# Performance work log

Measured on AMD Instinct MI355X. Metric: run time of the kernel, lower is better.

Reference implementation:

```python
import jax, jax.numpy as jnp
import numpy as np

EPS = 1e-5
SLOPE = 0.2

def _leaky(x):
    return jnp.where(x >= 0, x, SLOPE * x)

def _bn(x, g, b, axes):
    # batch-norm in training mode: biased stats over `axes`, per remaining channel dim
    mu = jnp.mean(x, axis=axes, keepdims=True)
    var = jnp.var(x, axis=axes, keepdims=True)
    shape = [1] * x.ndim
    shape[2 if x.ndim == 5 else 1] = -1
    return (x - mu) * jax.lax.rsqrt(var + EPS) * g.reshape(shape) + b.reshape(shape)

def setup_inputs() -> dict:
    key = jax.random.key(0)
    ks = jax.random.split(key, 6)
    T, B, C, H, W, D = 17, 16, 512, 16, 16, 256
    return {
        "cond": jax.random.normal(ks[0], (B, D), jnp.float32),
        "xbar": jax.random.normal(ks[1], (T, B, C, H, W), jnp.float32),
        "lin_w": jax.random.normal(ks[2], (D, D), jnp.float32) * 0.05,
        "lin_b": jnp.zeros((D,), jnp.float32),
        "bn_s_g": jnp.ones((D,), jnp.float32),
        "bn_s_b": jnp.zeros((D,), jnp.float32),
        "conv1_w": jax.random.normal(ks[3], (C, C), jnp.float32) * 0.05,
        "bn1_g": jnp.ones((C,), jnp.float32),
        "bn1_b": jnp.zeros((C,), jnp.float32),
        "conv2_w": jax.random.normal(ks[4], (C, C + D), jnp.float32) * 0.05,
        "bn2_g": jnp.ones((C,), jnp.float32),
        "bn2_b": jnp.zeros((C,), jnp.float32),
        "conv3_w": jax.random.normal(ks[5], (1, C, 2, 2), jnp.float32) * 0.05,
    }

def reference(cond, xbar, lin_w, lin_b, bn_s_g, bn_s_b, conv1_w, bn1_g, bn1_b, conv2_w, bn2_g, bn2_b, conv3_w):
    # sent_map: Linear -> BatchNorm1d (over batch) -> LeakyReLU
    sent = cond @ lin_w.T + lin_b                       # [B, D]
    sent = _leaky(_bn(sent, bn_s_g, bn_s_b, axes=(0,)))

    motions = xbar[1:] - xbar[:-1]                      # [F, B, C, H, W]
    F, B, C, H, W = motions.shape

    # motion_map: 1x1 conv -> BN (per-frame stats, matching the python loop) -> LeakyReLU
    h = jnp.einsum('fbchw,oc->fbohw', motions, conv1_w)
    h = _leaky(_bn(h, bn1_g, bn1_b, axes=(1, 3, 4)))

    # broadcast sentence vector over space (replaces per-pixel python loop)
    sent_dupe = jnp.broadcast_to(sent[None, :, :, None, None], (F, B, sent.shape[1], H, W))
    ms = jnp.concatenate([h, sent_dupe], axis=2)        # [F, B, C+D, H, W]

    # predictor: 1x1 conv -> BN (per-frame) -> LeakyReLU -> 2x2 stride-2 conv
    h2 = jnp.einsum('fbchw,oc->fbohw', ms, conv2_w)
    h2 = _leaky(_bn(h2, bn2_g, bn2_b, axes=(1, 3, 4)))

    h2f = h2.reshape(F * B, C, H, W)
    out = jax.lax.conv_general_dilated(
        h2f, conv3_w, window_strides=(2, 2), padding='VALID',
        dimension_numbers=('NCHW', 'OIHW', 'NCHW'))     # [F*B, 1, H/2, W/2]
    return out.reshape(F, B, -1)                        # matches view(B,-1) per frame + stack
```

## Files before the change

### kernel.cpp

```cpp
#include <hip/hip_runtime.h>
#include <hip/hip_bf16.h>

#define EPS 1e-5f
#define SLOPE 0.2f

#define NF 16
#define NBATCH 16
#define NC 512
#define NHW 256
#define ND 256
#define K2 768
#define MF 4096
#define FRAME_ELEMS ((size_t)MF * NC)

typedef __attribute__((ext_vector_type(8))) short short8;
typedef __attribute__((ext_vector_type(4))) float float4v;

__device__ __forceinline__ float lrelu(float v) { return v >= 0.f ? v : SLOPE * v; }
__device__ __forceinline__ float b2f(ushort u) { union { float f; uint i; } x; x.i = ((uint)u) << 16; return x.f; }
__device__ __forceinline__ ushort f2b(float f) {
  uint i = __float_as_uint(f);
  return (ushort)((i + 0x7FFFu + ((i >> 16) & 1u)) >> 16);
}
__device__ __forceinline__ void gl16(const ushort* g, ushort* l) {
  __builtin_amdgcn_global_load_lds(
      (const __attribute__((address_space(1))) unsigned int*)g,
      (__attribute__((address_space(3))) unsigned int*)l, 16, 0, 0);
}
#define SB __builtin_amdgcn_sched_barrier(0)

__global__ __launch_bounds__(256) void k_pre(
    const float* __restrict__ w1, const float* __restrict__ w2,
    const float* __restrict__ cond, const float* __restrict__ lin_w,
    const float* __restrict__ lin_b, const float* __restrict__ gam,
    const float* __restrict__ bet,
    ushort* __restrict__ w1b, ushort* __restrict__ w2b,
    float* __restrict__ bias2) {
  int bx = blockIdx.x, t = threadIdx.x;
  if (bx < 1024) {
    int i = bx * 256 + t;
    w1b[i] = f2b(w1[i]);
    int o = i >> 9, c = i & 511;
    w2b[i] = f2b(w2[(size_t)o * K2 + c]);
    return;
  }
  __shared__ float sl[NBATCH][ND];
  int d = t;
  {
    float acc[NBATCH];
    float bias = lin_b[d];
#pragma unroll
    for (int b = 0; b < NBATCH; ++b) acc[b] = bias;
    for (int k = 0; k < ND; ++k) {
      float w = lin_w[d * ND + k];
#pragma unroll
      for (int b = 0; b < NBATCH; ++b) acc[b] = fmaf(cond[b * ND + k], w, acc[b]);
    }
    float mu = 0.f;
#pragma unroll
    for (int b = 0; b < NBATCH; ++b) mu += acc[b];
    mu *= (1.f / NBATCH);
    float var = 0.f;
#pragma unroll
    for (int b = 0; b < NBATCH; ++b) { float x = acc[b] - mu; var = fmaf(x, x, var); }
    var *= (1.f / NBATCH);
    float sc = rsqrtf(var + EPS) * gam[d];
    float sh = bet[d] - mu * sc;
#pragma unroll
    for (int b = 0; b < NBATCH; ++b) sl[b][d] = lrelu(fmaf(acc[b], sc, sh));
  }
  __syncthreads();
  int o = (bx - 1024) * 256 + t;
  float acc2[NBATCH];
#pragma unroll
  for (int b = 0; b < NBATCH; ++b) acc2[b] = 0.f;
  for (int d2 = 0; d2 < ND; ++d2) {
    float wv = w2[(size_t)o * K2 + NC + d2];
#pragma unroll
    for (int b = 0; b < NBATCH; ++b) acc2[b] = fmaf(sl[b][d2], wv, acc2[b]);
  }
#pragma unroll
  for (int b = 0; b < NBATCH; ++b) bias2[b * NC + o] = acc2[b];
}

__device__ __forceinline__ void gemm_epi(
    float4v (&acc)[8][4], ushort* lds, const float* bias2, int has_bias,
    ushort* __restrict__ H, float2* __restrict__ part,
    int g, int bx, int n0, int w, int l, int wr, int wc) {
  int m0 = bx * 256;
  float bz[4];
#pragma unroll
  for (int fn = 0; fn < 4; ++fn)
    bz[fn] = has_bias ? bias2[bx * NC + n0 + wc * 64 + fn * 16 + (l & 15)] : 0.f;
  float sv[4], qv[4];
#pragma unroll
  for (int fn = 0; fn < 4; ++fn) {
    float s = 0.f, q = 0.f;
#pragma unroll
    for (int fm = 0; fm < 8; ++fm)
#pragma unroll
      for (int j = 0; j < 4; ++j) {
        float v = acc[fm][fn][j] + bz[fn];
        acc[fm][fn][j] = v;
        s += v;
        q = fmaf(v, v, q);
      }
    s += __shfl_xor(s, 16); s += __shfl_xor(s, 32);
    q += __shfl_xor(q, 16); q += __shfl_xor(q, 32);
    sv[fn] = s; qv[fn] = q;
  }
  if (l < 16) {
    int mb = bx * 2 + wr;
    float2* pp = part + ((size_t)g * 32 + mb) * NC + n0 + wc * 64 + l;
#pragma unroll
    for (int fn = 0; fn < 4; ++fn) pp[fn * 16] = make_float2(sv[fn], qv[fn]);
  }
  ushort* ep = &lds[w * 1088];
  ushort* Hg = H + ((size_t)g * MF + m0 + wr * 128) * NC + n0 + wc * 64;
#pragma unroll
  for (int fm = 0; fm < 8; ++fm) {
#pragma unroll
    for (int fn = 0; fn < 4; ++fn)
#pragma unroll
      for (int j = 0; j < 4; ++j)
        ep[((l >> 4) * 4 + j) * 68 + fn * 16 + (l & 15)] = f2b(acc[fm][fn][j]);
#pragma unroll
    for (int h = 0; h < 2; ++h) {
      int r = h * 8 + (l >> 3), sl = l & 7;
      short8 v = *(const short8*)&ep[r * 68 + sl * 8];
      *(short8*)&Hg[(size_t)(fm * 16 + r) * NC + sl * 8] = v;
    }
  }
}

__global__ __launch_bounds__(512, 2) void k_gemm1f(
    const float* __restrict__ xbar, const ushort* __restrict__ W,
    ushort* __restrict__ H, float2* __restrict__ part, int f0) {
  __shared__ ushort lds[65536];
  const int t = threadIdx.x, w = t >> 6, l = t & 63;
  const int g = blockIdx.z, bx = blockIdx.x, ny = blockIdx.y;
  const int n0 = ny * 256;
  const int wr = w >> 2, wc = w & 3;

  const ushort* Wg = W + (size_t)n0 * NC;
  size_t goff[4];
  int loff[4];
#pragma unroll
  for (int q = 0; q < 4; ++q) {
    int u = w * 256 + q * 64 + l;
    int row = u >> 3, cb = (u & 7) ^ (row & 7);
    goff[q] = (size_t)row * NC + cb * 8;
    loff[q] = u * 8;
  }
  const float* x0 = xbar + (((size_t)(f0 + g) * NBATCH + bx) * NC + w * 8) * NHW + l * 4;
  const float* x1 = x0 + (size_t)NBATCH * NC * NHW;

  int slot[2];
#pragma unroll
  for (int kk = 0; kk < 2; ++kk) slot[kk] = (((kk * 4 + (l >> 4)) ^ (l & 7)) * 8);
  const int swbase = w;

  float4 p0[4], p1[4];
#define AISSUE(h_, kt_)                                                      \
  do {                                                                       \
    _Pragma("unroll") for (int cc = 0; cc < 4; ++cc) {                       \
      size_t off = (size_t)((kt_) * 64 + (h_) * 4 + cc) * NHW;               \
      p1[cc] = *(const float4*)(x1 + off);                                   \
      p0[cc] = *(const float4*)(x0 + off);                                   \
    }                                                                        \
  } while (0)
#define ATRANS(h_, b_)                                                       \
  do {                                                                       \
    _Pragma("unroll") for (int i = 0; i < 4; ++i) {                          \
      int hw = l * 4 + i;                                                    \
      uint lo = (uint)f2b(((const float*)&p1[0])[i] - ((const float*)&p0[0])[i]) | \
                ((uint)f2b(((const float*)&p1[1])[i] - ((const float*)&p0[1])[i]) << 16); \
      uint hi = (uint)f2b(((const float*)&p1[2])[i] - ((const float*)&p0[2])[i]) | \
                ((uint)f2b(((const float*)&p1[3])[i] - ((const float*)&p0[3])[i]) << 16); \
      uint2 pk = make_uint2(lo, hi);                                         \
      *(uint2*)&lds[(b_) * 32768 + hw * 64 + ((swbase ^ (hw & 7)) * 8) + (h_) * 4] = pk; \
    }                                                                        \
  } while (0)
#define WSTAGE(t_, b_)                                                       \
  do {                                                                       \
    _Pragma("unroll") for (int q = 0; q < 4; ++q)                            \
        gl16(Wg + goff[q] + (t_) * 64, &lds[(b_) * 32768 + 16384 + loff[q]]); \
  } while (0)

  AISSUE(0, 0);
  WSTAGE(0, 0);
  WSTAGE(1, 1);
  asm volatile("s_waitcnt vmcnt(0)" ::: "memory"); SB;
  ATRANS(0, 0);
  AISSUE(1, 0);
  asm volatile("s_waitcnt vmcnt(0)" ::: "memory"); SB;
  ATRANS(1, 0);
  asm volatile("s_waitcnt lgkmcnt(0)" ::: "memory"); SB;
  __builtin_amdgcn_s_barrier(); SB;

  float4v acc[8][4];
#pragma unroll
  for (int i = 0; i < 8; ++i)
#pragma unroll
    for (int j = 0; j < 4; ++j) acc[i][j] = (float4v)0.f;

#pragma unroll
  for (int kt = 0; kt < 8; ++kt) {
    const int cur = kt & 1;
    const ushort* la = &lds[cur * 32768];
    const ushort* lb = la + 16384;
    if (kt < 7) AISSUE(0, kt + 1);
    short8 bf[4][2], af[4][2];
#pragma unroll
    for (int fn = 0; fn < 4; ++fn) {
      int r = wc * 64 + fn * 16 + (l & 15);
#pragma unroll
      for (int kk = 0; kk < 2; ++kk) bf[fn][kk] = *(const short8*)&lb[r * 64 + slot[kk]];
    }
#pragma unroll
    for (int fm = 0; fm < 4; ++fm) {
      int r = wr * 128 + fm * 16 + (l & 15);
#pragma unroll
      for (int kk = 0; kk < 2; ++kk) af[fm][kk] = *(const short8*)&la[r * 64 + slot[kk]];
    }
    asm volatile("s_waitcnt lgkmcnt(0)" ::: "memory"); SB;
    __builtin_amdgcn_s_setprio(1);
#pragma unroll
    for (int kk = 0; kk < 2; ++kk)
#pragma unroll
      for (int fm = 0; fm < 4; ++fm)
#pragma unroll
        for (int fn = 0; fn < 4; ++fn)
          acc[fm][fn] = __builtin_amdgcn_mfma_f32_16x16x32_bf16(
              af[fm][kk], bf[fn][kk], acc[fm][fn], 0, 0, 0);
    __builtin_amdgcn_s_setprio(0);
#pragma unroll
    for (int fm = 0; fm < 4; ++fm) {
      int r = wr * 128 + 64 + fm * 16 + (l & 15);
#pragma unroll
      for (int kk = 0; kk < 2; ++kk) af[fm][kk] = *(const short8*)&la[r * 64 + slot[kk]];
    }
    asm volatile("s_waitcnt lgkmcnt(0)" ::: "memory"); SB;
    __builtin_amdgcn_s_barrier(); SB;
    if (kt < 7) {
      asm volatile("s_waitcnt vmcnt(0)" ::: "memory"); SB;
      ATRANS(0, cur ^ 1);
      AISSUE(1, kt + 1);
      asm volatile("s_waitcnt vmcnt(0)" ::: "memory"); SB;
      ATRANS(1, cur ^ 1);
    }
    if (kt < 6) WSTAGE(kt + 2, cur);
    __builtin_amdgcn_s_setprio(1);
#pragma unroll
    for (int kk = 0; kk < 2; ++kk)
#pragma unroll
      for (int fm = 0; fm < 4; ++fm)
#pragma unroll
        for (int fn = 0; fn < 4; ++fn)
          acc[fm + 4][fn] = __builtin_amdgcn_mfma_f32_16x16x32_bf16(
              af[fm][kk], bf[fn][kk], acc[fm + 4][fn], 0, 0, 0);
    __builtin_amdgcn_s_setprio(0);
    if (kt < 7) {
      asm volatile("s_waitcnt lgkmcnt(0)" ::: "memory"); SB;
      __builtin_amdgcn_s_barrier(); SB;
    }
  }
#undef AISSUE
#undef ATRANS
#undef WSTAGE
  SB; __builtin_amdgcn_s_barrier(); SB;
  gemm_epi(acc, lds, nullptr, 0, H, part, g, bx, n0, w, l, wr, wc);
}

__global__ __launch_bounds__(512, 2) void k_gemm2f(
    const ushort* __restrict__ A, const ushort* __restrict__ W,
    const float2* __restrict__ st, const float* __restrict__ bias2,
    ushort* __restrict__ H, float2* __restrict__ part) {
  __shared__ ushort lds[65536];
  __shared__ float2 stl[NC];
  const int t = threadIdx.x, w = t >> 6, l = t & 63;
  const int g = blockIdx.z, bx = blockIdx.x, ny = blockIdx.y;
  const int m0 = bx * 256, n0 = ny * 256;
  const int wr = w >> 2, wc = w & 3;

  const ushort* Wg = W + (size_t)n0 * NC;
  const ushort* Ab = A + ((size_t)g * MF + m0) * NC;
  size_t goff[4], agoff[4];
  int loff[4], arow[4];
#pragma unroll
  for (int q = 0; q < 4; ++q) {
    int u = w * 256 + q * 64 + l;
    int row = u >> 3, cb = (u & 7) ^ (row & 7);
    goff[q] = (size_t)row * NC + cb * 8;
    loff[q] = u * 8;
    arow[q] = row;
    agoff[q] = (size_t)row * NC + (l & 7) * 8;
  }
  int slot[2];
#pragma unroll
  for (int kk = 0; kk < 2; ++kk) slot[kk] = (((kk * 4 + (l >> 4)) ^ (l & 7)) * 8);

  short8 ar[4];
  float2 sr[8];
#define A2ISSUE(kt_)                                                         \
  do {                                                                       \
    _Pragma("unroll") for (int q = 0; q < 4; ++q)                            \
        ar[q] = *(const short8*)(Ab + agoff[q] + (kt_) * 64);                \
  } while (0)
#define SRREAD(kt_)                                                          \
  do {                                                                       \
    _Pragma("unroll") for (int e = 0; e < 8; ++e)                            \
        sr[e] = stl[(kt_) * 64 + (l & 7) * 8 + e];                           \
  } while (0)
#define A2TRANS(b_)                                                          \
  do {                                                                       \
    _Pragma("unroll") for (int q = 0; q < 4; ++q) {                          \
      uint out[4];                                                           \
      _Pragma("unroll") for (int j = 0; j < 4; ++j) {                        \
        float xa = fmaf(b2f((ushort)ar[q][2 * j]), sr[2 * j].x, sr[2 * j].y); \
        float xb = fmaf(b2f((ushort)ar[q][2 * j + 1]), sr[2 * j + 1].x, sr[2 * j + 1].y); \
        xa = fmaxf(xa, SLOPE * xa);                                          \
        xb = fmaxf(xb, SLOPE * xb);                                          \
        out[j] = (uint)f2b(xa) | ((uint)f2b(xb) << 16);                      \
      }                                                                      \
      *(uint4*)&lds[(b_) * 32768 + arow[q] * 64 + (((l & 7) ^ (arow[q] & 7)) * 8)] = \
          *(const uint4*)out;                                                \
    }                                                                        \
  } while (0)
#define WSTAGE2(t_, b_)                                                      \
  do {                                                                       \
    _Pragma("unroll") for (int q = 0; q < 4; ++q)                            \
        gl16(Wg + goff[q] + (t_) * 64, &lds[(b_) * 32768 + 16384 + loff[q]]); \
  } while (0)

  stl[t] = st[(size_t)g * NC + t];
  if (t + 512 < NC) {}
  A2ISSUE(0);
  WSTAGE2(0, 0);
  WSTAGE2(1, 1);
  asm volatile("s_waitcnt lgkmcnt(0)" ::: "memory"); SB;
  __builtin_amdgcn_s_barrier(); SB;
  SRREAD(0);
  asm volatile("s_waitcnt vmcnt(0) lgkmcnt(0)" ::: "memory"); SB;
  A2TRANS(0);
  asm volatile("s_waitcnt lgkmcnt(0)" ::: "memory"); SB;
  __builtin_amdgcn_s_barrier(); SB;

  float4v acc[8][4];
#pragma unroll
  for (int i = 0; i < 8; ++i)
#pragma unroll
    for (int j = 0; j < 4; ++j) acc[i][j] = (float4v)0.f;

#pragma unroll
  for (int kt = 0; kt < 8; ++kt) {
    const int cur = kt & 1;
    const ushort* la = &lds[cur * 32768];
    const ushort* lb = la + 16384;
    if (kt < 7) A2ISSUE(kt + 1);
    short8 bf[4][2], af[4][2];
#pragma unroll
    for (int fn = 0; fn < 4; ++fn) {
      int r = wc * 64 + fn * 16 + (l & 15);
#pragma unroll
      for (int kk = 0; kk < 2; ++kk) bf[fn][kk] = *(const short8*)&lb[r * 64 + slot[kk]];
    }
#pragma unroll
    for (int fm = 0; fm < 4; ++fm) {
      int r = wr * 128 + fm * 16 + (l & 15);
#pragma unroll
      for (int kk = 0; kk < 2; ++kk) af[fm][kk] = *(const short8*)&la[r * 64 + slot[kk]];
    }
    asm volatile("s_waitcnt lgkmcnt(0)" ::: "memory"); SB;
    __builtin_amdgcn_s_setprio(1);
#pragma unroll
    for (int kk = 0; kk < 2; ++kk)
#pragma unroll
      for (int fm = 0; fm < 4; ++fm)
#pragma unroll
        for (int fn = 0; fn < 4; ++fn)
          acc[fm][fn] = __builtin_amdgcn_mfma_f32_16x16x32_bf16(
              af[fm][kk], bf[fn][kk], acc[fm][fn], 0, 0, 0);
    __builtin_amdgcn_s_setprio(0);
#pragma unroll
    for (int fm = 0; fm < 4; ++fm) {
      int r = wr * 128 + 64 + fm * 16 + (l & 15);
#pragma unroll
      for (int kk = 0; kk < 2; ++kk) af[fm][kk] = *(const short8*)&la[r * 64 + slot[kk]];
    }
    asm volatile("s_waitcnt lgkmcnt(0)" ::: "memory"); SB;
    __builtin_amdgcn_s_barrier(); SB;
    if (kt < 7) {
      SRREAD(kt + 1);
      asm volatile("s_waitcnt vmcnt(0) lgkmcnt(0)" ::: "memory"); SB;
      A2TRANS(cur ^ 1);
    }
    if (kt < 6) WSTAGE2(kt + 2, cur);
    __builtin_amdgcn_s_setprio(1);
#pragma unroll
    for (int kk = 0; kk < 2; ++kk)
#pragma unroll
      for (int fm = 0; fm < 4; ++fm)
#pragma unroll
        for (int fn = 0; fn < 4; ++fn)
          acc[fm + 4][fn] = __builtin_amdgcn_mfma_f32_16x16x32_bf16(
              af[fm][kk], bf[fn][kk], acc[fm + 4][fn], 0, 0, 0);
    __builtin_amdgcn_s_setprio(0);
    if (kt < 7) {
      asm volatile("s_waitcnt lgkmcnt(0)" ::: "memory"); SB;
      __builtin_amdgcn_s_barrier(); SB;
    }
  }
#undef A2ISSUE
#undef SRREAD
#undef A2TRANS
#undef WSTAGE2
  SB; __builtin_amdgcn_s_barrier(); SB;
  gemm_epi(acc, lds, bias2, 1, H, part, g, bx, n0, w, l, wr, wc);
}

__global__ __launch_bounds__(256) void k_stats2(
    const float2* __restrict__ part, const float* __restrict__ gam,
    const float* __restrict__ bet, float2* __restrict__ st) {
  int bi = blockIdx.x;
  int g = bi >> 1;
  int o = (bi & 1) * 256 + threadIdx.x;
  float s = 0.f, q = 0.f;
#pragma unroll
  for (int mb = 0; mb < 32; ++mb) {
    float2 v = part[((size_t)g * 32 + mb) * NC + o];
    s += v.x;
    q += v.y;
  }
  float mu = s * (1.f / 4096.f);
  float var = q * (1.f / 4096.f) - mu * mu;
  float sc = rsqrtf(var + EPS) * gam[o];
  st[g * NC + o] = make_float2(sc, bet[o] - mu * sc);
}

__global__ __launch_bounds__(256) void k_conv3(
    const ushort* __restrict__ h2, const float2* __restrict__ st2,
    const float* __restrict__ w3, float* __restrict__ out, int f0) {
  int g = blockIdx.z;
  int b = blockIdx.x >> 2;
  int q = blockIdx.x & 3;
  int t = threadIdx.x;
  int oi = q * 16 + (t >> 4);
  int cs = t & 15;
  int y = oi >> 3, x = oi & 7;
  const ushort* base = h2 + ((size_t)g * MF + b * NHW) * NC;
  int m00 = (2 * y) * 16 + 2 * x;
  float acc = 0.f;
#pragma unroll
  for (int c8 = cs * 32; c8 < cs * 32 + 32; c8 += 8) {
    short8 v0 = *(const short8*)&base[(size_t)(m00 + 0) * NC + c8];
    short8 v1 = *(const short8*)&base[(size_t)(m00 + 1) * NC + c8];
    short8 v2 = *(const short8*)&base[(size_t)(m00 + 16) * NC + c8];
    short8 v3 = *(const short8*)&base[(size_t)(m00 + 17) * NC + c8];
#pragma unroll
    for (int e = 0; e < 8; ++e) {
      float2 ss = st2[g * NC + c8 + e];
      float4 wv = ((const float4*)w3)[c8 + e];
      acc = fmaf(lrelu(fmaf(b2f((ushort)v0[e]), ss.x, ss.y)), wv.x, acc);
      acc = fmaf(lrelu(fmaf(b2f((ushort)v1[e]), ss.x, ss.y)), wv.y, acc);
      acc = fmaf(lrelu(fmaf(b2f((ushort)v2[e]), ss.x, ss.y)), wv.z, acc);
      acc = fmaf(lrelu(fmaf(b2f((ushort)v3[e]), ss.x, ss.y)), wv.w, acc);
    }
  }
  acc += __shfl_xor(acc, 1);
  acc += __shfl_xor(acc, 2);
  acc += __shfl_xor(acc, 4);
  acc += __shfl_xor(acc, 8);
  if (cs == 0) out[((size_t)(f0 + g) * NBATCH + b) * 64 + oi] = acc;
}

extern "C" void kernel_launch(void* const* d_in, const int* in_sizes, int n_in,
                              void* d_out, int out_size, void* d_ws, size_t ws_size,
                              hipStream_t stream) {
  const float* cond = (const float*)d_in[0];
  const float* xbar = (const float*)d_in[1];
  const float* lin_w = (const float*)d_in[2];
  const float* lin_b = (const float*)d_in[3];
  const float* bnsg = (const float*)d_in[4];
  const float* bnsb = (const float*)d_in[5];
  const float* w1 = (const float*)d_in[6];
  const float* bn1g = (const float*)d_in[7];
  const float* bn1b = (const float*)d_in[8];
  const float* w2 = (const float*)d_in[9];
  const float* bn2g = (const float*)d_in[10];
  const float* bn2b = (const float*)d_in[11];
  const float* w3 = (const float*)d_in[12];
  float* out = (float*)d_out;

  char* p = (char*)d_ws;
  float* bias2 = (float*)p;   p += ((NBATCH * NC * 4 + 255) & ~255);
  float2* st1 = (float2*)p;   p += ((NF * NC * 8 + 255) & ~255);
  float2* st2 = (float2*)p;   p += ((NF * NC * 8 + 255) & ~255);
  float2* part = (float2*)p;  p += (((size_t)NF * 32 * NC * 8 + 255) & ~255);
  ushort* w1b = (ushort*)p;   p += ((NC * NC * 2 + 255) & ~255);
  ushort* w2b = (ushort*)p;   p += ((NC * NC * 2 + 255) & ~255);
  size_t used = (size_t)(p - (char*)d_ws);
  const size_t frame_bytes = FRAME_ELEMS * 2;
  size_t rem = ws_size > used ? ws_size - used : 0;
  int FB = (int)(rem / (2 * frame_bytes));
  if (FB < 1) FB = 1;
  if (FB > NF) FB = NF;
  ushort* bufB = (ushort*)p;
  ushort* bufC = bufB + (size_t)FB * FRAME_ELEMS;

  k_pre<<<1026, 256, 0, stream>>>(w1, w2, cond, lin_w, lin_b, bnsg, bnsb,
                                  w1b, w2b, bias2);

  for (int f0 = 0; f0 < NF; f0 += FB) {
    int nb = (NF - f0) < FB ? (NF - f0) : FB;
    k_gemm1f<<<dim3(16, 2, nb), 512, 0, stream>>>(xbar, w1b, bufB, part, f0);
    k_stats2<<<2 * nb, 256, 0, stream>>>(part, bn1g, bn1b, st1);
    k_gemm2f<<<dim3(16, 2, nb), 512, 0, stream>>>(bufB, w2b, st1, bias2, bufC, part);
    k_stats2<<<2 * nb, 256, 0, stream>>>(part, bn2g, bn2b, st2);
    k_conv3<<<dim3(NBATCH * 4, 1, nb), 256, 0, stream>>>(bufC, st2, w3, out, f0);
  }
}
```

Before: 313.6 us.

## Split frame-difference transpose into separate kernel feeding a plain bf16 GEMM

Unfuses motion computation from the first GEMM. A new kernel computes consecutive-frame differences, converts them to bf16 and transposes them to channel-last, streaming each xbar frame once across a group of four frames instead of reading every frame twice. The first GEMM then loads both A and W tiles with direct global-to-LDS copies in a clean double-buffered pipeline, with no register transpose. The cost is an extra bf16 intermediate buffer written and read back, plus a third workspace buffer that may shrink the frame batch size.

```diff
diff --git a/kernel.cpp b/kernel.cpp
--- a/kernel.cpp
+++ b/kernel.cpp
@@ -83,6 +83,58 @@
   for (int b = 0; b < NBATCH; ++b) bias2[b * NC + o] = acc2[b];
 }
 
+__global__ __launch_bounds__(256) void k_mot(
+    const float* __restrict__ xbar, ushort* __restrict__ mot, int f0, int nb) {
+  __shared__ ushort T2[64][72];
+  int t = threadIdx.x;
+  int b = blockIdx.y;
+  int hw0 = (blockIdx.x & 3) * 64;
+  int c0 = (blockIdx.x >> 2) * 64;
+  int fg = blockIdx.z * 4;
+  int fe = fg + 4 < nb ? fg + 4 : nb;
+
+  int c4 = t >> 4;
+  int h16 = t & 15;
+  const size_t fstride = (size_t)NBATCH * NC * NHW;
+  const float* base = xbar + ((size_t)(f0 + fg) * NBATCH + b) * (NC * NHW) +
+                      (size_t)(c0 + c4 * 4) * NHW + hw0 + h16 * 4;
+
+  float4 prev[4], cur[4], nxt[4];
+#pragma unroll
+  for (int r = 0; r < 4; ++r) prev[r] = *(const float4*)(base + (size_t)r * NHW);
+#pragma unroll
+  for (int r = 0; r < 4; ++r) cur[r] = *(const float4*)(base + fstride + (size_t)r * NHW);
+
+  for (int fr = fg; fr < fe; ++fr) {
+    if (fr + 1 < fe) {
+      const float* xn = base + (size_t)(fr - fg + 2) * fstride;
+#pragma unroll
+      for (int r = 0; r < 4; ++r) nxt[r] = *(const float4*)(xn + (size_t)r * NHW);
+    }
+#pragma unroll
+    for (int i = 0; i < 4; ++i) {
+      ushort4 pk = make_ushort4(
+          f2b(((const float*)&cur[0])[i] - ((const float*)&prev[0])[i]),
+          f2b(((const float*)&cur[1])[i] - ((const float*)&prev[1])[i]),
+          f2b(((const float*)&cur[2])[i] - ((const float*)&prev[2])[i]),
+          f2b(((const float*)&cur[3])[i] - ((const float*)&prev[3])[i]));
+      *(ushort4*)&T2[h16 * 4 + i][c4 * 4] = pk;
+    }
+    __syncthreads();
+    ushort* mp = mot + ((size_t)fr * MF + b * NHW + hw0) * NC + c0;
+#pragma unroll
+    for (int it = 0; it < 2; ++it) {
+      int unit = it * 256 + t;
+      int hw = unit >> 3, q = unit & 7;
+      short8 v = *(const short8*)&T2[hw][q * 8];
+      *(short8*)&mp[(size_t)hw * NC + q * 8] = v;
+    }
+    __syncthreads();
+#pragma unroll
+    for (int r = 0; r < 4; ++r) { prev[r] = cur[r]; cur[r] = nxt[r]; }
+  }
+}
+
 __device__ __forceinline__ void gemm_epi(
     float4v (&acc)[8][4], ushort* lds, const float* bias2, int has_bias,
     ushort* __restrict__ H, float2* __restrict__ part,
@@ -133,16 +185,18 @@
   }
 }
 
-__global__ __launch_bounds__(512, 2) void k_gemm1f(
-    const float* __restrict__ xbar, const ushort* __restrict__ W,
-    ushort* __restrict__ H, float2* __restrict__ part, int f0) {
+__global__ __launch_bounds__(512, 2) void k_gemm8(
+    const ushort* __restrict__ A, const ushort* __restrict__ W,
+    ushort* __restrict__ H, float2* __restrict__ part) {
   __shared__ ushort lds[65536];
   const int t = threadIdx.x, w = t >> 6, l = t & 63;
   const int g = blockIdx.z, bx = blockIdx.x, ny = blockIdx.y;
-  const int n0 = ny * 256;
+  const int m0 = bx * 256, n0 = ny * 256;
   const int wr = w >> 2, wc = w & 3;
 
+  const ushort* Ag = A + (size_t)g * FRAME_ELEMS + (size_t)m0 * NC;
   const ushort* Wg = W + (size_t)n0 * NC;
+
   size_t goff[4];
   int loff[4];
 #pragma unroll
@@ -152,76 +206,50 @@
     goff[q] = (size_t)row * NC + cb * 8;
     loff[q] = u * 8;
   }
-  const float* x0 = xbar + (((size_t)(f0 + g) * NBATCH + bx) * NC + w * 8) * NHW + l * 4;
-  const float* x1 = x0 + (size_t)NBATCH * NC * NHW;
+
+#define STAGE8(t_, b_)                                               \
+  do {                                                               \
+    const int k0_ = (t_) * 64;                                       \
+    _Pragma("unroll") for (int q = 0; q < 4; ++q)                    \
+        gl16(Ag + goff[q] + k0_, &lds[(b_) * 32768 + loff[q]]);      \
+    _Pragma("unroll") for (int q = 0; q < 4; ++q)                    \
+        gl16(Wg + goff[q] + k0_, &lds[(b_) * 32768 + 16384 + loff[q]]); \
+  } while (0)
 
   int slot[2];
 #pragma unroll
   for (int kk = 0; kk < 2; ++kk) slot[kk] = (((kk * 4 + (l >> 4)) ^ (l & 7)) * 8);
-  const int swbase = w;
-
-  float4 p0[4], p1[4];
-#define AISSUE(h_, kt_)                                                      \
-  do {                                                                       \
-    _Pragma("unroll") for (int cc = 0; cc < 4; ++cc) {                       \
-      size_t off = (size_t)((kt_) * 64 + (h_) * 4 + cc) * NHW;               \
-      p1[cc] = *(const float4*)(x1 + off);                                   \
-      p0[cc] = *(const float4*)(x0 + off);                                   \
-    }                                                                        \
-  } while (0)
-#define ATRANS(h_, b_)                                                       \
-  do {                                                                       \
-    _Pragma("unroll") for (int i = 0; i < 4; ++i) {                          \
-      int hw = l * 4 + i;                                                    \
-      uint lo = (uint)f2b(((const float*)&p1[0])[i] - ((const float*)&p0[0])[i]) | \
-                ((uint)f2b(((const float*)&p1[1])[i] - ((const float*)&p0[1])[i]) << 16); \
-      uint hi = (uint)f2b(((const float*)&p1[2])[i] - ((const float*)&p0[2])[i]) | \
-                ((uint)f2b(((const float*)&p1[3])[i] - ((const float*)&p0[3])[i]) << 16); \
-      uint2 pk = make_uint2(lo, hi);                                         \
-      *(uint2*)&lds[(b_) * 32768 + hw * 64 + ((swbase ^ (hw & 7)) * 8) + (h_) * 4] = pk; \
-    }                                                                        \
-  } while (0)
-#define WSTAGE(t_, b_)                                                       \
-  do {                                                                       \
-    _Pragma("unroll") for (int q = 0; q < 4; ++q)                            \
-        gl16(Wg + goff[q] + (t_) * 64, &lds[(b_) * 32768 + 16384 + loff[q]]); \
-  } while (0)
-
-  AISSUE(0, 0);
-  WSTAGE(0, 0);
-  WSTAGE(1, 1);
-  asm volatile("s_waitcnt vmcnt(0)" ::: "memory"); SB;
-  ATRANS(0, 0);
-  AISSUE(1, 0);
-  asm volatile("s_waitcnt vmcnt(0)" ::: "memory"); SB;
-  ATRANS(1, 0);
-  asm volatile("s_waitcnt lgkmcnt(0)" ::: "memory"); SB;
+
+  float4v acc[8][4];
+#pragma unroll
+  for (int i = 0; i < 8; ++i)
+#pragma unroll
+    for (int j = 0; j < 4; ++j) acc[i][j] = (float4v)0.f;
+
+  STAGE8(0, 0);
+  STAGE8(1, 1);
+  asm volatile("s_waitcnt vmcnt(8)" ::: "memory"); SB;
   __builtin_amdgcn_s_barrier(); SB;
 
-  float4v acc[8][4];
-#pragma unroll
-  for (int i = 0; i < 8; ++i)
-#pragma unroll
-    for (int j = 0; j < 4; ++j) acc[i][j] = (float4v)0.f;
-
 #pragma unroll
   for (int kt = 0; kt < 8; ++kt) {
-    const int cur = kt & 1;
-    const ushort* la = &lds[cur * 32768];
+    const int b = kt & 1;
+    const ushort* la = &lds[b * 32768];
     const ushort* lb = la + 16384;
-    if (kt < 7) AISSUE(0, kt + 1);
     short8 bf[4][2], af[4][2];
 #pragma unroll
     for (int fn = 0; fn < 4; ++fn) {
       int r = wc * 64 + fn * 16 + (l & 15);
 #pragma unroll
-      for (int kk = 0; kk < 2; ++kk) bf[fn][kk] = *(const short8*)&lb[r * 64 + slot[kk]];
+      for (int kk = 0; kk < 2; ++kk)
+        bf[fn][kk] = *(const short8*)&lb[r * 64 + slot[kk]];
     }
 #pragma unroll
     for (int fm = 0; fm < 4; ++fm) {
       int r = wr * 128 + fm * 16 + (l & 15);
 #pragma unroll
-      for (int kk = 0; kk < 2; ++kk) af[fm][kk] = *(const short8*)&la[r * 64 + slot[kk]];
+      for (int kk = 0; kk < 2; ++kk)
+        af[fm][kk] = *(const short8*)&la[r * 64 + slot[kk]];
     }
     asm volatile("s_waitcnt lgkmcnt(0)" ::: "memory"); SB;
     __builtin_amdgcn_s_setprio(1);
@@ -238,18 +266,12 @@
     for (int fm = 0; fm < 4; ++fm) {
       int r = wr * 128 + 64 + fm * 16 + (l & 15);
 #pragma unroll
-      for (int kk = 0; kk < 2; ++kk) af[fm][kk] = *(const short8*)&la[r * 64 + slot[kk]];
+      for (int kk = 0; kk < 2; ++kk)
+        af[fm][kk] = *(const short8*)&la[r * 64 + slot[kk]];
     }
     asm volatile("s_waitcnt lgkmcnt(0)" ::: "memory"); SB;
     __builtin_amdgcn_s_barrier(); SB;
-    if (kt < 7) {
-      asm volatile("s_waitcnt vmcnt(0)" ::: "memory"); SB;
-      ATRANS(0, cur ^ 1);
-      AISSUE(1, kt + 1);
-      asm volatile("s_waitcnt vmcnt(0)" ::: "memory"); SB;
-      ATRANS(1, cur ^ 1);
-    }
-    if (kt < 6) WSTAGE(kt + 2, cur);
+    if (kt < 6) STAGE8(kt + 2, b);
     __builtin_amdgcn_s_setprio(1);
 #pragma unroll
     for (int kk = 0; kk < 2; ++kk)
@@ -261,13 +283,14 @@
               af[fm][kk], bf[fn][kk], acc[fm + 4][fn], 0, 0, 0);
     __builtin_amdgcn_s_setprio(0);
     if (kt < 7) {
-      asm volatile("s_waitcnt lgkmcnt(0)" ::: "memory"); SB;
+      if (kt < 6) asm volatile("s_waitcnt vmcnt(8)" ::: "memory");
+      else        asm volatile("s_waitcnt vmcnt(0)" ::: "memory");
+      SB;
       __builtin_amdgcn_s_barrier(); SB;
     }
   }
-#undef AISSUE
-#undef ATRANS
-#undef WSTAGE
+#undef STAGE8
+
   SB; __builtin_amdgcn_s_barrier(); SB;
   gemm_epi(acc, lds, nullptr, 0, H, part, g, bx, n0, w, l, wr, wc);
 }
@@ -334,7 +357,6 @@
   } while (0)
 
   stl[t] = st[(size_t)g * NC + t];
-  if (t + 512 < NC) {}
   A2ISSUE(0);
   WSTAGE2(0, 0);
   WSTAGE2(1, 1);
@@ -502,10 +524,11 @@
   size_t used = (size_t)(p - (char*)d_ws);
   const size_t frame_bytes = FRAME_ELEMS * 2;
   size_t rem = ws_size > used ? ws_size - used : 0;
-  int FB = (int)(rem / (2 * frame_bytes));
+  int FB = (int)(rem / (3 * frame_bytes));
   if (FB < 1) FB = 1;
   if (FB > NF) FB = NF;
-  ushort* bufB = (ushort*)p;
+  ushort* bufA = (ushort*)p;
+  ushort* bufB = bufA + (size_t)FB * FRAME_ELEMS;
   ushort* bufC = bufB + (size_t)FB * FRAME_ELEMS;
 
   k_pre<<<1026, 256, 0, stream>>>(w1, w2, cond, lin_w, lin_b, bnsg, bnsb,
@@ -513,7 +536,9 @@
 
   for (int f0 = 0; f0 < NF; f0 += FB) {
     int nb = (NF - f0) < FB ? (NF - f0) : FB;
-    k_gemm1f<<<dim3(16, 2, nb), 512, 0, stream>>>(xbar, w1b, bufB, part, f0);
+    int ngrp = (nb + 3) / 4;
+    k_mot<<<dim3(32, NBATCH, ngrp), 256, 0, stream>>>(xbar, bufA, f0, nb);
+    k_gemm8<<<dim3(16, 2, nb), 512, 0, stream>>>(bufA, w1b, bufB, part);
     k_stats2<<<2 * nb, 256, 0, stream>>>(part, bn1g, bn1b, st1);
     k_gemm2f<<<dim3(16, 2, nb), 512, 0, stream>>>(bufB, w2b, st1, bias2, bufC, part);
     k_stats2<<<2 * nb, 256, 0, stream>>>(part, bn2g, bn2b, st2);
```

After: 271.2 us. 13.5% less time.

## Restructure GEMM pipelines for deeper prefetch and single-barrier iterations

Applied to the files above, without the earlier changes.

Both GEMM kernels now prefetch the A operand two k-tiles ahead in registers (double register buffers in gemm2, a full 64-channel tile per ALD in gemm1), stage W one tile ahead instead of two, and drop the mid-iteration barrier, using partial vmcnt waits. gemm1 also changes its thread-to-channel/pixel mapping and swaps grid axes so the two N-blocks of the same frame/batch launch adjacently, which may improve L2 reuse of xbar. Launch bounds drop to 1 block per CU minimum, allowing more registers at the risk of lower occupancy.

```diff
diff --git a/kernel.cpp b/kernel.cpp
--- a/kernel.cpp
+++ b/kernel.cpp
@@ -133,13 +133,13 @@
   }
 }
 
-__global__ __launch_bounds__(512, 2) void k_gemm1f(
+__global__ __launch_bounds__(512, 1) void k_gemm1m(
     const float* __restrict__ xbar, const ushort* __restrict__ W,
     ushort* __restrict__ H, float2* __restrict__ part, int f0) {
   __shared__ ushort lds[65536];
   const int t = threadIdx.x, w = t >> 6, l = t & 63;
-  const int g = blockIdx.z, bx = blockIdx.x, ny = blockIdx.y;
-  const int n0 = ny * 256;
+  const int g = blockIdx.z, bx = blockIdx.y;
+  const int n0 = blockIdx.x * 256;
   const int wr = w >> 2, wc = w & 3;
 
   const ushort* Wg = W + (size_t)n0 * NC;
@@ -152,64 +152,65 @@
     goff[q] = (size_t)row * NC + cb * 8;
     loff[q] = u * 8;
   }
-  const float* x0 = xbar + (((size_t)(f0 + g) * NBATCH + bx) * NC + w * 8) * NHW + l * 4;
-  const float* x1 = x0 + (size_t)NBATCH * NC * NHW;
+#define WST(t_, b_)                                                      \
+  do {                                                                   \
+    _Pragma("unroll") for (int q = 0; q < 4; ++q)                        \
+        gl16(Wg + goff[q] + (t_) * 64, &lds[(b_) * 32768 + 16384 + loff[q]]); \
+  } while (0)
+
+  const int c4 = (t >> 3) & 15;
+  const int hh = ((t >> 7) << 3) + (t & 7);
+  const float* xb0 = xbar + ((size_t)(f0 + g) * NBATCH + bx) * (NC * NHW);
+  const float* xb1 = xb0 + (size_t)NBATCH * NC * NHW;
+
+  float4 pA[2][2][4];
+#define ALD(kt_)                                                         \
+  do {                                                                   \
+    _Pragma("unroll") for (int u = 0; u < 2; ++u)                        \
+      _Pragma("unroll") for (int cc = 0; cc < 4; ++cc) {                 \
+        size_t co = (size_t)((kt_) * 64 + c4 * 4 + cc) * NHW + hh * 4 + u * 128; \
+        pA[u][0][cc] = *(const float4*)(xb1 + co);                       \
+        pA[u][1][cc] = *(const float4*)(xb0 + co);                       \
+      }                                                                  \
+  } while (0)
+#define ATRANS(b_)                                                       \
+  do {                                                                   \
+    _Pragma("unroll") for (int u = 0; u < 2; ++u)                        \
+      _Pragma("unroll") for (int i = 0; i < 4; ++i) {                    \
+        int hw = hh * 4 + i + u * 128;                                   \
+        uint lo = (uint)f2b(((const float*)&pA[u][0][0])[i] - ((const float*)&pA[u][1][0])[i]) | \
+                  ((uint)f2b(((const float*)&pA[u][0][1])[i] - ((const float*)&pA[u][1][1])[i]) << 16); \
+        uint hi = (uint)f2b(((const float*)&pA[u][0][2])[i] - ((const float*)&pA[u][1][2])[i]) | \
+                  ((uint)f2b(((const float*)&pA[u][0][3])[i] - ((const float*)&pA[u][1][3])[i]) << 16); \
+        *(uint2*)&lds[(b_) * 32768 + hw * 64 + (((c4 >> 1) ^ (hw & 7)) * 8) + (c4 & 1) * 4] = \
+            make_uint2(lo, hi);                                          \
+      }                                                                  \
+  } while (0)
 
   int slot[2];
 #pragma unroll
   for (int kk = 0; kk < 2; ++kk) slot[kk] = (((kk * 4 + (l >> 4)) ^ (l & 7)) * 8);
-  const int swbase = w;
-
-  float4 p0[4], p1[4];
-#define AISSUE(h_, kt_)                                                      \
-  do {                                                                       \
-    _Pragma("unroll") for (int cc = 0; cc < 4; ++cc) {                       \
-      size_t off = (size_t)((kt_) * 64 + (h_) * 4 + cc) * NHW;               \
-      p1[cc] = *(const float4*)(x1 + off);                                   \
-      p0[cc] = *(const float4*)(x0 + off);                                   \
-    }                                                                        \
-  } while (0)
-#define ATRANS(h_, b_)                                                       \
-  do {                                                                       \
-    _Pragma("unroll") for (int i = 0; i < 4; ++i) {                          \
-      int hw = l * 4 + i;                                                    \
-      uint lo = (uint)f2b(((const float*)&p1[0])[i] - ((const float*)&p0[0])[i]) | \
-                ((uint)f2b(((const float*)&p1[1])[i] - ((const float*)&p0[1])[i]) << 16); \
-      uint hi = (uint)f2b(((const float*)&p1[2])[i] - ((const float*)&p0[2])[i]) | \
-                ((uint)f2b(((const float*)&p1[3])[i] - ((const float*)&p0[3])[i]) << 16); \
-      uint2 pk = make_uint2(lo, hi);                                         \
-      *(uint2*)&lds[(b_) * 32768 + hw * 64 + ((swbase ^ (hw & 7)) * 8) + (h_) * 4] = pk; \
-    }                                                                        \
-  } while (0)
-#define WSTAGE(t_, b_)                                                       \
-  do {                                                                       \
-    _Pragma("unroll") for (int q = 0; q < 4; ++q)                            \
-        gl16(Wg + goff[q] + (t_) * 64, &lds[(b_) * 32768 + 16384 + loff[q]]); \
-  } while (0)
-
-  AISSUE(0, 0);
-  WSTAGE(0, 0);
-  WSTAGE(1, 1);
-  asm volatile("s_waitcnt vmcnt(0)" ::: "memory"); SB;
-  ATRANS(0, 0);
-  AISSUE(1, 0);
-  asm volatile("s_waitcnt vmcnt(0)" ::: "memory"); SB;
-  ATRANS(1, 0);
+
+  float4v acc[8][4];
+#pragma unroll
+  for (int i = 0; i < 8; ++i)
+#pragma unroll
+    for (int j = 0; j < 4; ++j) acc[i][j] = (float4v)0.f;
+
+  ALD(0);
+  WST(0, 0);
+  asm volatile("s_waitcnt vmcnt(4)" ::: "memory"); SB;
+  ATRANS(0);
+  ALD(1);
   asm volatile("s_waitcnt lgkmcnt(0)" ::: "memory"); SB;
+  asm volatile("s_waitcnt vmcnt(16)" ::: "memory"); SB;
   __builtin_amdgcn_s_barrier(); SB;
-
-  float4v acc[8][4];
-#pragma unroll
-  for (int i = 0; i < 8; ++i)
-#pragma unroll
-    for (int j = 0; j < 4; ++j) acc[i][j] = (float4v)0.f;
 
 #pragma unroll
   for (int kt = 0; kt < 8; ++kt) {
     const int cur = kt & 1;
     const ushort* la = &lds[cur * 32768];
     const ushort* lb = la + 16384;
-    if (kt < 7) AISSUE(0, kt + 1);
     short8 bf[4][2], af[4][2];
 #pragma unroll
     for (int fn = 0; fn < 4; ++fn) {
@@ -241,15 +242,12 @@
       for (int kk = 0; kk < 2; ++kk) af[fm][kk] = *(const short8*)&la[r * 64 + slot[kk]];
     }
     asm volatile("s_waitcnt lgkmcnt(0)" ::: "memory"); SB;
-    __builtin_amdgcn_s_barrier(); SB;
     if (kt < 7) {
       asm volatile("s_waitcnt vmcnt(0)" ::: "memory"); SB;
-      ATRANS(0, cur ^ 1);
-      AISSUE(1, kt + 1);
-      asm volatile("s_waitcnt vmcnt(0)" ::: "memory"); SB;
-      ATRANS(1, cur ^ 1);
-    }
-    if (kt < 6) WSTAGE(kt + 2, cur);
+      ATRANS(cur ^ 1);
+      WST(kt + 1, cur ^ 1);
+      if (kt < 6) ALD(kt + 2);
+    }
     __builtin_amdgcn_s_setprio(1);
 #pragma unroll
     for (int kk = 0; kk < 2; ++kk)
@@ -262,17 +260,20 @@
     __builtin_amdgcn_s_setprio(0);
     if (kt < 7) {
       asm volatile("s_waitcnt lgkmcnt(0)" ::: "memory"); SB;
+      if (kt < 6) asm volatile("s_waitcnt vmcnt(16)" ::: "memory");
+      else        asm volatile("s_waitcnt vmcnt(0)" ::: "memory");
+      SB;
       __builtin_amdgcn_s_barrier(); SB;
     }
   }
-#undef AISSUE
+#undef ALD
 #undef ATRANS
-#undef WSTAGE
+#undef WST
   SB; __builtin_amdgcn_s_barrier(); SB;
   gemm_epi(acc, lds, nullptr, 0, H, part, g, bx, n0, w, l, wr, wc);
 }
 
-__global__ __launch_bounds__(512, 2) void k_gemm2f(
+__global__ __launch_bounds__(512, 1) void k_gemm2f(
     const ushort* __restrict__ A, const ushort* __restrict__ W,
     const float2* __restrict__ st, const float* __restrict__ bias2,
     ushort* __restrict__ H, float2* __restrict__ part) {
@@ -300,50 +301,50 @@
 #pragma unroll
   for (int kk = 0; kk < 2; ++kk) slot[kk] = (((kk * 4 + (l >> 4)) ^ (l & 7)) * 8);
 
-  short8 ar[4];
+  short8 ar0[4], ar1[4];
   float2 sr[8];
-#define A2ISSUE(kt_)                                                         \
-  do {                                                                       \
-    _Pragma("unroll") for (int q = 0; q < 4; ++q)                            \
-        ar[q] = *(const short8*)(Ab + agoff[q] + (kt_) * 64);                \
-  } while (0)
-#define SRREAD(kt_)                                                          \
-  do {                                                                       \
-    _Pragma("unroll") for (int e = 0; e < 8; ++e)                            \
-        sr[e] = stl[(kt_) * 64 + (l & 7) * 8 + e];                           \
-  } while (0)
-#define A2TRANS(b_)                                                          \
-  do {                                                                       \
-    _Pragma("unroll") for (int q = 0; q < 4; ++q) {                          \
-      uint out[4];                                                           \
-      _Pragma("unroll") for (int j = 0; j < 4; ++j) {                        \
-        float xa = fmaf(b2f((ushort)ar[q][2 * j]), sr[2 * j].x, sr[2 * j].y); \
-        float xb = fmaf(b2f((ushort)ar[q][2 * j + 1]), sr[2 * j + 1].x, sr[2 * j + 1].y); \
-        xa = fmaxf(xa, SLOPE * xa);                                          \
-        xb = fmaxf(xb, SLOPE * xb);                                          \
-        out[j] = (uint)f2b(xa) | ((uint)f2b(xb) << 16);                      \
-      }                                                                      \
+#define A2LD(kt_, dst)                                                   \
+  do {                                                                   \
+    _Pragma("unroll") for (int q = 0; q < 4; ++q)                        \
+        dst[q] = *(const short8*)(Ab + agoff[q] + (kt_) * 64);           \
+  } while (0)
+#define SRREAD(kt_)                                                      \
+  do {                                                                   \
+    _Pragma("unroll") for (int e = 0; e < 8; ++e)                        \
+        sr[e] = stl[(kt_) * 64 + (l & 7) * 8 + e];                       \
+  } while (0)
+#define A2TRANS(src, b_)                                                 \
+  do {                                                                   \
+    _Pragma("unroll") for (int q = 0; q < 4; ++q) {                      \
+      uint out[4];                                                       \
+      _Pragma("unroll") for (int j = 0; j < 4; ++j) {                    \
+        float xa = fmaf(b2f((ushort)src[q][2 * j]), sr[2 * j].x, sr[2 * j].y); \
+        float xb = fmaf(b2f((ushort)src[q][2 * j + 1]), sr[2 * j + 1].x, sr[2 * j + 1].y); \
+        xa = fmaxf(xa, SLOPE * xa);                                      \
+        xb = fmaxf(xb, SLOPE * xb);                                      \
+        out[j] = (uint)f2b(xa) | ((uint)f2b(xb) << 16);                  \
+      }                                                                  \
       *(uint4*)&lds[(b_) * 32768 + arow[q] * 64 + (((l & 7) ^ (arow[q] & 7)) * 8)] = \
-          *(const uint4*)out;                                                \
-    }                                                                        \
-  } while (0)
-#define WSTAGE2(t_, b_)                                                      \
-  do {                                                                       \
-    _Pragma("unroll") for (int q = 0; q < 4; ++q)                            \
+          *(const uint4*)out;                                            \
+    }                                                                    \
+  } while (0)
+#define WST2(t_, b_)                                                     \
+  do {                                                                   \
+    _Pragma("unroll") for (int q = 0; q < 4; ++q)                        \
         gl16(Wg + goff[q] + (t_) * 64, &lds[(b_) * 32768 + 16384 + loff[q]]); \
   } while (0)
 
   stl[t] = st[(size_t)g * NC + t];
-  if (t + 512 < NC) {}
-  A2ISSUE(0);
-  WSTAGE2(0, 0);
-  WSTAGE2(1, 1);
+  A2LD(0, ar0);
+  WST2(0, 0);
+  A2LD(1, ar1);
+  __syncthreads();
+  SRREAD(0);
+  asm volatile("s_waitcnt vmcnt(8)" ::: "memory"); SB;
   asm volatile("s_waitcnt lgkmcnt(0)" ::: "memory"); SB;
-  __builtin_amdgcn_s_barrier(); SB;
-  SRREAD(0);
-  asm volatile("s_waitcnt vmcnt(0) lgkmcnt(0)" ::: "memory"); SB;
-  A2TRANS(0);
+  A2TRANS(ar0, 0);
   asm volatile("s_waitcnt lgkmcnt(0)" ::: "memory"); SB;
+  asm volatile("s_waitcnt vmcnt(4)" ::: "memory"); SB;
   __builtin_amdgcn_s_barrier(); SB;
 
   float4v acc[8][4];
@@ -357,7 +358,7 @@
     const int cur = kt & 1;
     const ushort* la = &lds[cur * 32768];
     const ushort* lb = la + 16384;
-    if (kt < 7) A2ISSUE(kt + 1);
+    if (kt < 7) SRREAD(kt + 1);
     short8 bf[4][2], af[4][2];
 #pragma unroll
     for (int fn = 0; fn < 4; ++fn) {
@@ -389,13 +390,12 @@
       for (int kk = 0; kk < 2; ++kk) af[fm][kk] = *(const short8*)&la[r * 64 + slot[kk]];
     }
     asm volatile("s_waitcnt lgkmcnt(0)" ::: "memory"); SB;
-    __builtin_amdgcn_s_barrier(); SB;
     if (kt < 7) {
-      SRREAD(kt + 1);
-      asm volatile("s_waitcnt vmcnt(0) lgkmcnt(0)" ::: "memory"); SB;
-      A2TRANS(cur ^ 1);
-    }
-    if (kt < 6) WSTAGE2(kt + 2, cur);
+      asm volatile("s_waitcnt vmcnt(0)" ::: "memory"); SB;
+      if ((kt & 1) == 0) A2TRANS(ar1, cur ^ 1); else A2TRANS(ar0, cur ^ 1);
+      WST2(kt + 1, cur ^ 1);
+      if (kt < 6) { if ((kt & 1) == 0) A2LD(kt + 2, ar0); else A2LD(kt + 2, ar1); }
+    }
     __builtin_amdgcn_s_setprio(1);
 #pragma unroll
     for (int kk = 0; kk < 2; ++kk)
@@ -408,13 +408,16 @@
     __builtin_amdgcn_s_setprio(0);
     if (kt < 7) {
       asm volatile("s_waitcnt lgkmcnt(0)" ::: "memory"); SB;
+      if (kt < 6) asm volatile("s_waitcnt vmcnt(4)" ::: "memory");
+      else        asm volatile("s_waitcnt vmcnt(0)" ::: "memory");
+      SB;
       __builtin_amdgcn_s_barrier(); SB;
     }
   }
-#undef A2ISSUE
+#undef A2LD
 #undef SRREAD
 #undef A2TRANS
-#undef WSTAGE2
+#undef WST2
   SB; __builtin_amdgcn_s_barrier(); SB;
   gemm_epi(acc, lds, bias2, 1, H, part, g, bx, n0, w, l, wr, wc);
 }
@@ -513,7 +516,7 @@
 
   for (int f0 = 0; f0 < NF; f0 += FB) {
     int nb = (NF - f0) < FB ? (NF - f0) : FB;
-    k_gemm1f<<<dim3(16, 2, nb), 512, 0, stream>>>(xbar, w1b, bufB, part, f0);
+    k_gemm1m<<<dim3(2, 16, nb), 512, 0, stream>>>(xbar, w1b, bufB, part, f0);
     k_stats2<<<2 * nb, 256, 0, stream>>>(part, bn1g, bn1b, st1);
     k_gemm2f<<<dim3(16, 2, nb), 512, 0, stream>>>(bufB, w2b, st1, bias2, bufC, part);
     k_stats2<<<2 * nb, 256, 0, stream>>>(part, bn2g, bn2b, st2);
```

Result: slower. 450.1 us (+43.5%).
